# Kernel tuning notes

Measured on AMD Instinct MI355X. Metric: run time of the kernel, lower is better.

The kernel has to match this reference:

```python
import jax, jax.numpy as jnp
import numpy as np
from jax.scipy.special import logsumexp

N = 512   # hidden states (obs_number)
M = 256   # emission symbols == sequence length (raw_number)
B = 128   # batch


def setup_inputs() -> dict:
    key = jax.random.key(0)
    k1, k2, k3, k4 = jax.random.split(key, 4)
    return {
        "obs": jax.random.randint(k1, (B, M), 0, M),
        "unnormalized_state_priors": jax.random.normal(k2, (N,), dtype=jnp.float32),
        "unnormalized_transition_matrix": jax.random.normal(k3, (N, N), dtype=jnp.float32),
        "unnormalized_emission_matrix": jax.random.normal(k4, (N, M), dtype=jnp.float32),
    }


def reference(obs, unnormalized_state_priors, unnormalized_transition_matrix,
              unnormalized_emission_matrix):
    # Normalized matrices are computed ONCE (the torch code redundantly
    # recomputes them every timestep; the math is identical).
    log_priors = jax.nn.log_softmax(unnormalized_state_priors)                 # [N]
    log_T = jax.nn.log_softmax(unnormalized_transition_matrix, axis=0)         # [N,N], T[i,k]=P(i|k)
    log_E = jax.nn.log_softmax(unnormalized_emission_matrix, axis=1)           # [N,M]

    # Emission log-probs per timestep: em[b,t,i] = log_E[i, obs[b,t]] -> [B,M,N]
    em = jnp.moveaxis(log_E[:, obs], 0, -1)

    alpha0 = em[:, 0, :] + log_priors                                          # [B,N]

    def step(a_prev, e_t):
        # log-domain matmul: a[b,i] = logsumexp_k( log_T[i,k] + a_prev[b,k] )
        a = e_t + logsumexp(log_T[None, :, :] + a_prev[:, None, :], axis=-1)   # [B,N]
        return a, logsumexp(a, axis=-1)                                        # carry, per-t log-sum

    em_tm = jnp.swapaxes(em, 0, 1)                                             # time-major [M,B,N]
    _, ls_rest = jax.lax.scan(step, alpha0, em_tm[1:])                         # [M-1,B]

    ls0 = logsumexp(alpha0, axis=-1)                                           # [B]
    log_sums = jnp.concatenate([ls0[:, None], ls_rest.T], axis=1)              # [B,M]
    return log_sums
```

## Files before the change

### kernel.cpp

```cpp
#include <hip/hip_runtime.h>
#include <hip/hip_bf16.h>
#include <math.h>

#define NN 512
#define MM 256
#define BB 128

typedef float        f32x4 __attribute__((ext_vector_type(4)));
typedef unsigned int u32;
typedef u32          u32x2 __attribute__((ext_vector_type(2)));
typedef unsigned long long u64;
typedef int          i32x8 __attribute__((ext_vector_type(8)));

#define LOG16F 2.772588722239781f
#define SCL1   0x7F

__device__ __forceinline__ float wave_max(float v) {
#pragma unroll
    for (int o = 32; o > 0; o >>= 1) v = fmaxf(v, __shfl_xor(v, o));
    return v;
}
__device__ __forceinline__ float wave_sum(float v) {
#pragma unroll
    for (int o = 32; o > 0; o >>= 1) v += __shfl_xor(v, o);
    return v;
}


__global__ void k_col_lse(const float* __restrict__ T, float* __restrict__ c) {
    int k = blockIdx.x, j = threadIdx.x;
    float m = -INFINITY, s = 0.f;
#pragma unroll
    for (int q = 0; q < 8; ++q) {
        float x = T[(q * 64 + j) * NN + k];
        if (x > m) { s = s * __expf(m - x) + 1.f; m = x; }
        else       { s += __expf(x - m); }
    }
    float mw = wave_max(m);
    float sw = wave_sum(s * __expf(m - mw));
    if (j == 0) c[k] = mw + __logf(sw);
}

__global__ void k_rowM(const float* __restrict__ T, const float* __restrict__ c,
                       float* __restrict__ M) {
    int i = blockIdx.x, j = threadIdx.x;
    float mx = -INFINITY;
#pragma unroll
    for (int d = 0; d < 8; ++d) {
        int k = j * 8 + d;
        mx = fmaxf(mx, T[i * NN + k] - c[k]);
    }
    mx = wave_max(mx);
    if (j == 0) M[i] = mx - __logf(64.f);
}

__global__ void k_prep(const float* __restrict__ T, const float* __restrict__ c,
                       const float* __restrict__ M, const float* __restrict__ pr,
                       const float* __restrict__ E,
                       float* __restrict__ lp2, u32* __restrict__ PA,
                       float* __restrict__ EX) {
    int blk = blockIdx.x, l = threadIdx.x;
    if (blk < 512) {
        float mm = -INFINITY;
#pragma unroll
        for (int q = 0; q < 8; ++q) mm = fmaxf(mm, M[q * 64 + l]);
        float CMv = wave_max(mm);
        int i = blk;
        float v[4];
        float mx = -INFINITY;
#pragma unroll
        for (int d = 0; d < 4; ++d) {
            v[d] = E[i * MM + l * 4 + d];
            mx = fmaxf(mx, v[d]);
        }
        mx = wave_max(mx);
        float s = 0.f;
#pragma unroll
        for (int d = 0; d < 4; ++d) s += __expf(v[d] - mx);
        s = wave_sum(s);
        float lse = mx + __logf(s);
        float add = M[i] - CMv - LOG16F - lse;
#pragma unroll
        for (int d = 0; d < 4; ++d)
            EX[(size_t)(l * 4 + d) * NN + i] = __expf(v[d] + add);
    } else if (blk < 640) {
        int bb = blk - 512;
        int tile = bb >> 2, kc = bb & 3;
        int row = tile * 16 + (l & 15);
        int kb  = kc * 128 + (l >> 4) * 32;
        float Mi = M[row];
        i32x8 dd;
#pragma unroll
        for (int q = 0; q < 8; ++q) {
            float p0 = __expf(T[row * NN + kb + 4*q + 0] - c[kb + 4*q + 0] - Mi);
            float p1 = __expf(T[row * NN + kb + 4*q + 1] - c[kb + 4*q + 1] - Mi);
            float p2 = __expf(T[row * NN + kb + 4*q + 2] - c[kb + 4*q + 2] - Mi);
            float p3 = __expf(T[row * NN + kb + 4*q + 3] - c[kb + 4*q + 3] - Mi);
            int d = 0;
            d = __builtin_amdgcn_cvt_pk_fp8_f32(p0, p1, d, false);
            d = __builtin_amdgcn_cvt_pk_fp8_f32(p2, p3, d, true);
            dd[q] = d;
        }
        *(i32x8*)(PA + ((size_t)bb * 64 + l) * 8) = dd;
    } else {
        float mm = -INFINITY;
#pragma unroll
        for (int q = 0; q < 8; ++q) mm = fmaxf(mm, M[q * 64 + l]);
        float CMv = wave_max(mm);
        float x[8];
        float mx = -INFINITY;
#pragma unroll
        for (int q = 0; q < 8; ++q) {
            x[q] = pr[q * 64 + l];
            mx = fmaxf(mx, x[q]);
        }
        mx = wave_max(mx);
        float s = 0.f;
#pragma unroll
        for (int q = 0; q < 8; ++q) s += __expf(x[q] - mx);
        s = wave_sum(s);
        float lse = mx + __logf(s);
#pragma unroll
        for (int q = 0; q < 8; ++q) {
            int i = q * 64 + l;
            lp2[i] = __expf(x[q] - lse - M[i] + CMv + LOG16F);
        }
    }
}

__global__ __launch_bounds__(512, 2) void k_scan(
        const int* __restrict__ obs, const float* __restrict__ lp2,
        const float* __restrict__ Mrow, const u32* __restrict__ PAu,
        const float* __restrict__ EX, float* __restrict__ out) {
    int b = blockIdx.x, tid = threadIdx.x;
    int w = tid >> 6, l = tid & 63;
    int h32 = (l >> 4) * 32;
    int r4 = (l >> 4) * 4;
    __shared__ unsigned char us8[NN] __attribute__((aligned(64)));
    __shared__ float rB[8] __attribute__((aligned(16)));
    __shared__ float outs[MM] __attribute__((aligned(16)));
    __shared__ int obs_s[MM];
    if (tid < MM) obs_s[tid] = obs[b * MM + tid];

    float mm = -INFINITY;
#pragma unroll
    for (int q = 0; q < 8; ++q) mm = fmaxf(mm, Mrow[q * 64 + l]);
    float C_M = wave_max(mm);

    i32x8 pa[16];
#pragma unroll
    for (int ti = 0; ti < 4; ++ti)
#pragma unroll
        for (int kc = 0; kc < 4; ++kc)
            pa[ti * 4 + kc] = *(const i32x8*)(PAu
                + ((size_t)(((w * 4 + ti) * 4 + kc) * 64) + l) * 8);
#pragma unroll
    for (int q = 0; q < 16; ++q) asm volatile("" : "+a"(pa[q]));

    int ubase[4];
#pragma unroll
    for (int ti = 0; ti < 4; ++ti) ubase[ti] = (w * 4 + ti) * 16 + r4;
    __syncthreads();

    int o0 = obs_s[0];
    f32x4 e4[4];
    float loc = 0.f;
#pragma unroll
    for (int ti = 0; ti < 4; ++ti) {
        f32x4 ex  = *(const f32x4*)(EX  + (size_t)o0 * NN + (w * 4 + ti) * 16 + r4);
        f32x4 lpv = *(const f32x4*)(lp2 + (w * 4 + ti) * 16 + r4);
#pragma unroll
        for (int r = 0; r < 4; ++r) {
            float e = ex[r] * lpv[r];
            e4[ti][r] = e; loc += e;
        }
    }
    loc += __shfl_xor(loc, 16);
    loc += __shfl_xor(loc, 32);
    if (l == 0) rB[w] = loc;
    __syncthreads();
    f32x4 sv0 = *(const f32x4*)rB;
    f32x4 sv1 = *(const f32x4*)(rB + 4);
    float S = (sv0[0] + sv0[1]) + (sv0[2] + sv0[3])
            + (sv1[0] + sv1[1]) + (sv1[2] + sv1[3]);
    S = fmaxf(S, 1e-35f);
    float sc = __builtin_amdgcn_rcpf(S) * 16.f;
    if ((l & 15) == 0) {
#pragma unroll
        for (int ti = 0; ti < 4; ++ti) {
            int d = 0;
            d = __builtin_amdgcn_cvt_pk_fp8_f32(e4[ti][0] * sc, e4[ti][1] * sc, d, false);
            d = __builtin_amdgcn_cvt_pk_fp8_f32(e4[ti][2] * sc, e4[ti][3] * sc, d, true);
            *(u32*)&us8[ubase[ti]] = (u32)d;
        }
    }
    __syncthreads();
    float lS = __logf(S);
    if (tid == 0) outs[0] = lS;
    float K = C_M + lS;

#pragma unroll 1
    for (int t = 1; t < MM; ++t) {
        int o = obs_s[t];
        f32x4 ex[4];
#pragma unroll
        for (int ti = 0; ti < 4; ++ti)
            ex[ti] = *(const f32x4*)(EX + (size_t)o * NN + (w * 4 + ti) * 16 + r4);

        const unsigned char* ub = us8;
        f32x4 a0 = {0.f,0.f,0.f,0.f}, a1 = {0.f,0.f,0.f,0.f};
        f32x4 a2 = {0.f,0.f,0.f,0.f}, a3 = {0.f,0.f,0.f,0.f};
        f32x4 b0 = {0.f,0.f,0.f,0.f}, b1 = {0.f,0.f,0.f,0.f};
        f32x4 b2 = {0.f,0.f,0.f,0.f}, b3 = {0.f,0.f,0.f,0.f};
        __builtin_amdgcn_s_setprio(1);
#pragma unroll
        for (int kc = 0; kc < 2; ++kc) {
            i32x8 bbA = *(const i32x8*)(ub + kc * 128 + h32);
            i32x8 bbB = *(const i32x8*)(ub + (kc + 2) * 128 + h32);
            a0 = __builtin_amdgcn_mfma_scale_f32_16x16x128_f8f6f4(
                     pa[0 * 4 + kc], bbA, a0, 0, 0, 0, SCL1, 0, SCL1);
            a1 = __builtin_amdgcn_mfma_scale_f32_16x16x128_f8f6f4(
                     pa[1 * 4 + kc], bbA, a1, 0, 0, 0, SCL1, 0, SCL1);
            a2 = __builtin_amdgcn_mfma_scale_f32_16x16x128_f8f6f4(
                     pa[2 * 4 + kc], bbA, a2, 0, 0, 0, SCL1, 0, SCL1);
            a3 = __builtin_amdgcn_mfma_scale_f32_16x16x128_f8f6f4(
                     pa[3 * 4 + kc], bbA, a3, 0, 0, 0, SCL1, 0, SCL1);
            b0 = __builtin_amdgcn_mfma_scale_f32_16x16x128_f8f6f4(
                     pa[0 * 4 + kc + 2], bbB, b0, 0, 0, 0, SCL1, 0, SCL1);
            b1 = __builtin_amdgcn_mfma_scale_f32_16x16x128_f8f6f4(
                     pa[1 * 4 + kc + 2], bbB, b1, 0, 0, 0, SCL1, 0, SCL1);
            b2 = __builtin_amdgcn_mfma_scale_f32_16x16x128_f8f6f4(
                     pa[2 * 4 + kc + 2], bbB, b2, 0, 0, 0, SCL1, 0, SCL1);
            b3 = __builtin_amdgcn_mfma_scale_f32_16x16x128_f8f6f4(
                     pa[3 * 4 + kc + 2], bbB, b3, 0, 0, 0, SCL1, 0, SCL1);
        }
        __builtin_amdgcn_s_setprio(0);
        f32x4 sacc[4] = { a0 + b0, a1 + b1, a2 + b2, a3 + b3 };

        loc = 0.f;
#pragma unroll
        for (int ti = 0; ti < 4; ++ti)
#pragma unroll
            for (int r = 0; r < 4; ++r) {
                float e = ex[ti][r] * sacc[ti][r];
                e4[ti][r] = e; loc += e;
            }
        loc += __shfl_xor(loc, 16);
        loc += __shfl_xor(loc, 32);
        if (l == 0) rB[w] = loc;
        __syncthreads();
        sv0 = *(const f32x4*)rB;
        sv1 = *(const f32x4*)(rB + 4);
        S = (sv0[0] + sv0[1]) + (sv0[2] + sv0[3])
          + (sv1[0] + sv1[1]) + (sv1[2] + sv1[3]);
        S = fmaxf(S, 1e-35f);
        sc = __builtin_amdgcn_rcpf(S) * 16.f;
        if ((l & 15) == 0) {
#pragma unroll
            for (int ti = 0; ti < 4; ++ti) {
                int d = 0;
                d = __builtin_amdgcn_cvt_pk_fp8_f32(e4[ti][0] * sc, e4[ti][1] * sc, d, false);
                d = __builtin_amdgcn_cvt_pk_fp8_f32(e4[ti][2] * sc, e4[ti][3] * sc, d, true);
                *(u32*)&us8[ubase[ti]] = (u32)d;
            }
        }
        __syncthreads();
        float lSn = __logf(S);
        if (tid == 0) outs[t] = K + lSn;
        K += C_M + lSn;
    }

    __syncthreads();
    if (tid < MM) out[(size_t)b * MM + tid] = outs[tid];
}

extern "C" void kernel_launch(void* const* d_in, const int* in_sizes, int n_in,
                              void* d_out, int out_size, void* d_ws, size_t ws_size,
                              hipStream_t stream) {
    const int*   obs = (const int*)d_in[0];
    const float* pri = (const float*)d_in[1];
    const float* T   = (const float*)d_in[2];
    const float* E   = (const float*)d_in[3];
    float* out = (float*)d_out;
    char* ws = (char*)d_ws;

    float* c   = (float*)(ws + 0);
    float* lp2 = (float*)(ws + 2048);
    float* M   = (float*)(ws + 4096);
    u32*   PA  = (u32*)(ws + 8192);
    float* EX  = (float*)(ws + 8192 + 256 * 1024);

    k_col_lse<<<512, 64, 0, stream>>>(T, c);
    k_rowM   <<<512, 64, 0, stream>>>(T, c, M);
    k_prep   <<<641, 64, 0, stream>>>(T, c, M, pri, E, lp2, PA, EX);
    k_scan   <<<BB, 512, 0, stream>>>(obs, lp2, M, PA, EX, out);
}
```

Baseline: 344.4 us.

## Interleave two batch sequences per block to overlap MFMA with reductions

Each workgroup now handles two batch rows and staggers them by half a step. The MFMA matmul for one sequence is issued while the other sequence's normalization and fp8 requantization finishes, and the two streams share a single barrier per half-step. This is meant to hide the serial reduce/sync latency of the per-timestep recurrence and to reuse the register-resident transition matrix across two sequences. In exchange, only 64 blocks are launched instead of 128, so fewer CUs are used. Outputs are also written directly to global memory instead of being staged through shared memory.

```diff
diff --git a/kernel.cpp b/kernel.cpp
--- a/kernel.cpp
+++ b/kernel.cpp
@@ -128,19 +128,90 @@
     }
 }
 
+#define MFMA_BLOCK(UB, SACC)                                                     \
+    {                                                                            \
+        f32x4 _a0={0.f,0.f,0.f,0.f}, _a1={0.f,0.f,0.f,0.f};                      \
+        f32x4 _a2={0.f,0.f,0.f,0.f}, _a3={0.f,0.f,0.f,0.f};                      \
+        f32x4 _b0={0.f,0.f,0.f,0.f}, _b1={0.f,0.f,0.f,0.f};                      \
+        f32x4 _b2={0.f,0.f,0.f,0.f}, _b3={0.f,0.f,0.f,0.f};                      \
+        __builtin_amdgcn_s_setprio(1);                                           \
+        _Pragma("unroll")                                                        \
+        for (int kc = 0; kc < 2; ++kc) {                                         \
+            i32x8 bbA = *(const i32x8*)((UB) + kc * 128 + h32);                  \
+            i32x8 bbB = *(const i32x8*)((UB) + (kc + 2) * 128 + h32);            \
+            _a0 = __builtin_amdgcn_mfma_scale_f32_16x16x128_f8f6f4(pa[0*4+kc],   bbA, _a0, 0,0,0, SCL1, 0, SCL1); \
+            _a1 = __builtin_amdgcn_mfma_scale_f32_16x16x128_f8f6f4(pa[1*4+kc],   bbA, _a1, 0,0,0, SCL1, 0, SCL1); \
+            _a2 = __builtin_amdgcn_mfma_scale_f32_16x16x128_f8f6f4(pa[2*4+kc],   bbA, _a2, 0,0,0, SCL1, 0, SCL1); \
+            _a3 = __builtin_amdgcn_mfma_scale_f32_16x16x128_f8f6f4(pa[3*4+kc],   bbA, _a3, 0,0,0, SCL1, 0, SCL1); \
+            _b0 = __builtin_amdgcn_mfma_scale_f32_16x16x128_f8f6f4(pa[0*4+kc+2], bbB, _b0, 0,0,0, SCL1, 0, SCL1); \
+            _b1 = __builtin_amdgcn_mfma_scale_f32_16x16x128_f8f6f4(pa[1*4+kc+2], bbB, _b1, 0,0,0, SCL1, 0, SCL1); \
+            _b2 = __builtin_amdgcn_mfma_scale_f32_16x16x128_f8f6f4(pa[2*4+kc+2], bbB, _b2, 0,0,0, SCL1, 0, SCL1); \
+            _b3 = __builtin_amdgcn_mfma_scale_f32_16x16x128_f8f6f4(pa[3*4+kc+2], bbB, _b3, 0,0,0, SCL1, 0, SCL1); \
+        }                                                                        \
+        __builtin_amdgcn_s_setprio(0);                                           \
+        SACC[0] = _a0 + _b0; SACC[1] = _a1 + _b1;                                \
+        SACC[2] = _a2 + _b2; SACC[3] = _a3 + _b3;                                \
+    }
+
+#define EX_LOAD(DST, O)                                                          \
+    {                                                                            \
+        const float* _exr = EX + (size_t)(O) * NN;                               \
+        _Pragma("unroll")                                                        \
+        for (int ti = 0; ti < 4; ++ti)                                           \
+            DST[ti] = *(const f32x4*)(_exr + (w * 4 + ti) * 16 + r4);            \
+    }
+
+#define REDUCE_S2(E4, EXV, SACC, RBUF)                                           \
+    {                                                                            \
+        float _loc = 0.f;                                                        \
+        _Pragma("unroll")                                                        \
+        for (int ti = 0; ti < 4; ++ti)                                           \
+            _Pragma("unroll")                                                    \
+            for (int r = 0; r < 4; ++r) {                                        \
+                float _e = EXV[ti][r] * SACC[ti][r];                             \
+                E4[ti][r] = _e; _loc += _e;                                      \
+            }                                                                    \
+        _loc += __shfl_xor(_loc, 16);                                            \
+        _loc += __shfl_xor(_loc, 32);                                            \
+        if (l == 0) RBUF[w] = _loc;                                              \
+    }
+
+#define FINISH_S3(E4, RBUF, UBUF, LSN)                                           \
+    {                                                                            \
+        f32x4 _s0 = *(const f32x4*)(RBUF);                                       \
+        f32x4 _s1 = *(const f32x4*)((RBUF) + 4);                                 \
+        f32x4 _ss = _s0 + _s1;                                                   \
+        float _S = (_ss[0] + _ss[1]) + (_ss[2] + _ss[3]);                        \
+        _S = fmaxf(_S, 1e-35f);                                                  \
+        float _sc = __builtin_amdgcn_rcpf(_S) * 16.f;                            \
+        if ((l & 15) == 0) {                                                     \
+            _Pragma("unroll")                                                    \
+            for (int ti = 0; ti < 4; ++ti) {                                     \
+                int _d = 0;                                                      \
+                _d = __builtin_amdgcn_cvt_pk_fp8_f32(E4[ti][0] * _sc, E4[ti][1] * _sc, _d, false); \
+                _d = __builtin_amdgcn_cvt_pk_fp8_f32(E4[ti][2] * _sc, E4[ti][3] * _sc, _d, true);  \
+                *(u32*)&(UBUF)[ubase[ti]] = (u32)_d;                             \
+            }                                                                    \
+        }                                                                        \
+        LSN = __logf(_S);                                                        \
+    }
+
 __global__ __launch_bounds__(512, 2) void k_scan(
         const int* __restrict__ obs, const float* __restrict__ lp2,
         const float* __restrict__ Mrow, const u32* __restrict__ PAu,
         const float* __restrict__ EX, float* __restrict__ out) {
-    int b = blockIdx.x, tid = threadIdx.x;
+    int blk = blockIdx.x, tid = threadIdx.x;
+    int bA = blk * 2, bB = blk * 2 + 1;
     int w = tid >> 6, l = tid & 63;
     int h32 = (l >> 4) * 32;
     int r4 = (l >> 4) * 4;
-    __shared__ unsigned char us8[NN] __attribute__((aligned(64)));
-    __shared__ float rB[8] __attribute__((aligned(16)));
-    __shared__ float outs[MM] __attribute__((aligned(16)));
-    __shared__ int obs_s[MM];
-    if (tid < MM) obs_s[tid] = obs[b * MM + tid];
+    __shared__ unsigned char usA[NN] __attribute__((aligned(64)));
+    __shared__ unsigned char usB[NN] __attribute__((aligned(64)));
+    __shared__ float rA_[8] __attribute__((aligned(16)));
+    __shared__ float rB_[8] __attribute__((aligned(16)));
+    __shared__ int obs_s[2][MM];
+    if (tid < MM) obs_s[0][tid] = obs[(size_t)bA * MM + tid];
+    else          obs_s[1][tid - MM] = obs[(size_t)bB * MM + (tid - MM)];
 
     float mm = -INFINITY;
 #pragma unroll
@@ -162,116 +233,69 @@
     for (int ti = 0; ti < 4; ++ti) ubase[ti] = (w * 4 + ti) * 16 + r4;
     __syncthreads();
 
-    int o0 = obs_s[0];
-    f32x4 e4[4];
-    float loc = 0.f;
-#pragma unroll
-    for (int ti = 0; ti < 4; ++ti) {
-        f32x4 ex  = *(const f32x4*)(EX  + (size_t)o0 * NN + (w * 4 + ti) * 16 + r4);
-        f32x4 lpv = *(const f32x4*)(lp2 + (w * 4 + ti) * 16 + r4);
-#pragma unroll
-        for (int r = 0; r < 4; ++r) {
-            float e = ex[r] * lpv[r];
-            e4[ti][r] = e; loc += e;
-        }
-    }
-    loc += __shfl_xor(loc, 16);
-    loc += __shfl_xor(loc, 32);
-    if (l == 0) rB[w] = loc;
+    f32x4 e4A[4], e4B[4], exv[4];
+    {
+        int oA = obs_s[0][0];
+        EX_LOAD(exv, oA);
+        f32x4 lpv[4];
+#pragma unroll
+        for (int ti = 0; ti < 4; ++ti)
+            lpv[ti] = *(const f32x4*)(lp2 + (w * 4 + ti) * 16 + r4);
+        f32x4 sac0[4];
+#pragma unroll
+        for (int ti = 0; ti < 4; ++ti) sac0[ti] = lpv[ti];
+        REDUCE_S2(e4A, exv, sac0, rA_);
+        int oB = obs_s[1][0];
+        EX_LOAD(exv, oB);
+        REDUCE_S2(e4B, exv, sac0, rB_);
+    }
     __syncthreads();
-    f32x4 sv0 = *(const f32x4*)rB;
-    f32x4 sv1 = *(const f32x4*)(rB + 4);
-    float S = (sv0[0] + sv0[1]) + (sv0[2] + sv0[3])
-            + (sv1[0] + sv1[1]) + (sv1[2] + sv1[3]);
-    S = fmaxf(S, 1e-35f);
-    float sc = __builtin_amdgcn_rcpf(S) * 16.f;
-    if ((l & 15) == 0) {
-#pragma unroll
-        for (int ti = 0; ti < 4; ++ti) {
-            int d = 0;
-            d = __builtin_amdgcn_cvt_pk_fp8_f32(e4[ti][0] * sc, e4[ti][1] * sc, d, false);
-            d = __builtin_amdgcn_cvt_pk_fp8_f32(e4[ti][2] * sc, e4[ti][3] * sc, d, true);
-            *(u32*)&us8[ubase[ti]] = (u32)d;
-        }
-    }
+    float lSA, lSB, KA, KB;
+    FINISH_S3(e4A, rA_, usA, lSA);
+    if (tid == 0) out[(size_t)bA * MM + 0] = lSA;
+    KA = C_M + lSA;
+    f32x4 exA[4], exB[4];
+    EX_LOAD(exA, obs_s[0][1]);
     __syncthreads();
-    float lS = __logf(S);
-    if (tid == 0) outs[0] = lS;
-    float K = C_M + lS;
+
+    f32x4 sacc[4];
 
 #pragma unroll 1
     for (int t = 1; t < MM; ++t) {
-        int o = obs_s[t];
-        f32x4 ex[4];
-#pragma unroll
-        for (int ti = 0; ti < 4; ++ti)
-            ex[ti] = *(const f32x4*)(EX + (size_t)o * NN + (w * 4 + ti) * 16 + r4);
-
-        const unsigned char* ub = us8;
-        f32x4 a0 = {0.f,0.f,0.f,0.f}, a1 = {0.f,0.f,0.f,0.f};
-        f32x4 a2 = {0.f,0.f,0.f,0.f}, a3 = {0.f,0.f,0.f,0.f};
-        f32x4 b0 = {0.f,0.f,0.f,0.f}, b1 = {0.f,0.f,0.f,0.f};
-        f32x4 b2 = {0.f,0.f,0.f,0.f}, b3 = {0.f,0.f,0.f,0.f};
-        __builtin_amdgcn_s_setprio(1);
-#pragma unroll
-        for (int kc = 0; kc < 2; ++kc) {
-            i32x8 bbA = *(const i32x8*)(ub + kc * 128 + h32);
-            i32x8 bbB = *(const i32x8*)(ub + (kc + 2) * 128 + h32);
-            a0 = __builtin_amdgcn_mfma_scale_f32_16x16x128_f8f6f4(
-                     pa[0 * 4 + kc], bbA, a0, 0, 0, 0, SCL1, 0, SCL1);
-            a1 = __builtin_amdgcn_mfma_scale_f32_16x16x128_f8f6f4(
-                     pa[1 * 4 + kc], bbA, a1, 0, 0, 0, SCL1, 0, SCL1);
-            a2 = __builtin_amdgcn_mfma_scale_f32_16x16x128_f8f6f4(
-                     pa[2 * 4 + kc], bbA, a2, 0, 0, 0, SCL1, 0, SCL1);
-            a3 = __builtin_amdgcn_mfma_scale_f32_16x16x128_f8f6f4(
-                     pa[3 * 4 + kc], bbA, a3, 0, 0, 0, SCL1, 0, SCL1);
-            b0 = __builtin_amdgcn_mfma_scale_f32_16x16x128_f8f6f4(
-                     pa[0 * 4 + kc + 2], bbB, b0, 0, 0, 0, SCL1, 0, SCL1);
-            b1 = __builtin_amdgcn_mfma_scale_f32_16x16x128_f8f6f4(
-                     pa[1 * 4 + kc + 2], bbB, b1, 0, 0, 0, SCL1, 0, SCL1);
-            b2 = __builtin_amdgcn_mfma_scale_f32_16x16x128_f8f6f4(
-                     pa[2 * 4 + kc + 2], bbB, b2, 0, 0, 0, SCL1, 0, SCL1);
-            b3 = __builtin_amdgcn_mfma_scale_f32_16x16x128_f8f6f4(
-                     pa[3 * 4 + kc + 2], bbB, b3, 0, 0, 0, SCL1, 0, SCL1);
-        }
-        __builtin_amdgcn_s_setprio(0);
-        f32x4 sacc[4] = { a0 + b0, a1 + b1, a2 + b2, a3 + b3 };
-
-        loc = 0.f;
-#pragma unroll
-        for (int ti = 0; ti < 4; ++ti)
-#pragma unroll
-            for (int r = 0; r < 4; ++r) {
-                float e = ex[ti][r] * sacc[ti][r];
-                e4[ti][r] = e; loc += e;
-            }
-        loc += __shfl_xor(loc, 16);
-        loc += __shfl_xor(loc, 32);
-        if (l == 0) rB[w] = loc;
+        MFMA_BLOCK(usA, sacc);
+        if (t == 1) {
+            FINISH_S3(e4B, rB_, usB, lSB);
+            if (tid == 0) out[(size_t)bB * MM + 0] = lSB;
+            KB = C_M + lSB;
+        } else {
+            FINISH_S3(e4B, rB_, usB, lSB);
+            if (tid == 0) out[(size_t)bB * MM + (t - 1)] = KB + lSB;
+            KB += C_M + lSB;
+        }
+        REDUCE_S2(e4A, exA, sacc, rA_);
+        EX_LOAD(exB, obs_s[1][t]);
         __syncthreads();
-        sv0 = *(const f32x4*)rB;
-        sv1 = *(const f32x4*)(rB + 4);
-        S = (sv0[0] + sv0[1]) + (sv0[2] + sv0[3])
-          + (sv1[0] + sv1[1]) + (sv1[2] + sv1[3]);
+
+        MFMA_BLOCK(usB, sacc);
+        {
+            FINISH_S3(e4A, rA_, usA, lSA);
+            if (tid == 0) out[(size_t)bA * MM + t] = KA + lSA;
+            KA += C_M + lSA;
+        }
+        REDUCE_S2(e4B, exB, sacc, rB_);
+        EX_LOAD(exA, obs_s[0][(t + 1 < MM) ? t + 1 : t]);
+        __syncthreads();
+    }
+
+    {
+        f32x4 s0 = *(const f32x4*)rB_;
+        f32x4 s1 = *(const f32x4*)(rB_ + 4);
+        f32x4 ss = s0 + s1;
+        float S = (ss[0] + ss[1]) + (ss[2] + ss[3]);
         S = fmaxf(S, 1e-35f);
-        sc = __builtin_amdgcn_rcpf(S) * 16.f;
-        if ((l & 15) == 0) {
-#pragma unroll
-            for (int ti = 0; ti < 4; ++ti) {
-                int d = 0;
-                d = __builtin_amdgcn_cvt_pk_fp8_f32(e4[ti][0] * sc, e4[ti][1] * sc, d, false);
-                d = __builtin_amdgcn_cvt_pk_fp8_f32(e4[ti][2] * sc, e4[ti][3] * sc, d, true);
-                *(u32*)&us8[ubase[ti]] = (u32)d;
-            }
-        }
-        __syncthreads();
         float lSn = __logf(S);
-        if (tid == 0) outs[t] = K + lSn;
-        K += C_M + lSn;
-    }
-
-    __syncthreads();
-    if (tid < MM) out[(size_t)b * MM + tid] = outs[tid];
+        if (tid == 0) out[(size_t)bB * MM + (MM - 1)] = KB + lSn;
+    }
 }
 
 extern "C" void kernel_launch(void* const* d_in, const int* in_sizes, int n_in,
@@ -293,5 +317,5 @@
     k_col_lse<<<512, 64, 0, stream>>>(T, c);
     k_rowM   <<<512, 64, 0, stream>>>(T, c, M);
     k_prep   <<<641, 64, 0, stream>>>(T, c, M, pri, E, lp2, PA, EX);
-    k_scan   <<<BB, 512, 0, stream>>>(obs, lp2, M, PA, EX, out);
-}
+    k_scan   <<<BB / 2, 512, 0, stream>>>(obs, lp2, M, PA, EX, out);
+}
```

After: 820.9 us. 2.38x slower.
